# Kernel optimization log

Measured on AMD Instinct MI355X. Metric: run time of the kernel, lower is better.

The kernel has to match this reference:

```python
import jax, jax.numpy as jnp
import numpy as np

PAD = 2  # matches init_kwargs padding

# HEALPix face layout (DLWP-HEALPix / earth2grid convention):
#   faces 0-3 : northern polar cap
#   faces 4-7 : equatorial belt
#   faces 8-11: southern polar cap
# Padding each face gathers edge strips from topological neighbor faces;
# polar-cap neighbors require 90/180-degree rotations, and the two degenerate
# equatorial corners (touching a pole vertex, 3 faces meet) are filled with
# edge continuations + an averaged corner pixel.

def _rot(x, k):
    return jnp.rot90(x, k, axes=(-2, -1))

def _corner_tl(t, l, p):
    # degenerate top-left corner of an equatorial face (pole vertex)
    shp = t.shape[:-2] + (p, p)
    c = jnp.zeros(shp, t.dtype)
    c = c.at[..., :, -1].set(t[..., -p:, 0])          # continue top neighbor's left edge
    c = c.at[..., -1, :].set(l[..., 0, -p:])          # continue left neighbor's top edge
    c = c.at[..., -1, -1].set(0.5 * t[..., -1, 0] + 0.5 * l[..., 0, -1])
    return c

def _corner_br(b, r, p):
    # degenerate bottom-right corner of an equatorial face (pole vertex)
    shp = b.shape[:-2] + (p, p)
    c = jnp.zeros(shp, b.dtype)
    c = c.at[..., :, 0].set(b[..., :p, -1])
    c = c.at[..., 0, :].set(r[..., -1, :p])
    c = c.at[..., 0, 0].set(0.5 * b[..., 0, -1] + 0.5 * r[..., -1, 0])
    return c

def _assemble(tl, t, tr, l, c, r, bl, b, br):
    top = jnp.concatenate([tl, t, tr], axis=-1)
    mid = jnp.concatenate([l, c, r], axis=-1)
    bot = jnp.concatenate([bl, b, br], axis=-1)
    return jnp.concatenate([top, mid, bot], axis=-2)

def _pn(c, t, tl, l, bl, b, br, r, tr, p):
    # northern polar face: top/left neighbors are rotated polar faces
    return _assemble(
        _rot(tl, 2)[..., -p:, -p:], _rot(t, 1)[..., -p:, :], _rot(tr, 1)[..., -p:, :p],
        _rot(l, -1)[..., :, -p:],   c,                       r[..., :, :p],
        bl[..., :p, -p:],           b[..., :p, :],           br[..., :p, :p])

def _pe(c, t, tl, l, bl, b, br, r, tr, p):
    # equatorial face: no rotations; tl/br are precomputed degenerate corners
    return _assemble(
        tl,               t[..., -p:, :], tr[..., -p:, :p],
        l[..., :, -p:],   c,              r[..., :, :p],
        bl[..., :p, -p:], b[..., :p, :],  br)

def _ps(c, t, tl, l, bl, b, br, r, tr, p):
    # southern polar face: mirror image of the northern case
    return _assemble(
        tl[..., -p:, :p], t[..., -p:, :],        tr[..., -p:, -p:],
        l[..., :, -p:],   c,                     _rot(r, -1)[..., :, :p],
        _rot(bl, 1)[..., :p, -p:], _rot(b, 1)[..., :p, :], _rot(br, 2)[..., :p, :p])

def healpix_pad(x, p):
    # x: (B, 12, C, H, W) -> (B, 12, C, H+2p, W+2p)
    f = [x[:, i] for i in range(12)]
    out = []
    for i in range(4):  # northern cap faces 0..3
        out.append(_pn(f[i], t=f[(i + 1) % 4], tl=f[(i + 2) % 4], l=f[(i - 1) % 4],
                       bl=f[(i - 1) % 4], b=f[4 + i], br=f[8 + i],
                       r=f[4 + (i + 1) % 4], tr=f[(i + 1) % 4], p=p))
    for i in range(4):  # equatorial faces 4..7
        out.append(_pe(f[4 + i], t=f[i], tl=_corner_tl(f[i], f[(i - 1) % 4], p),
                       l=f[(i - 1) % 4], bl=f[4 + (i - 1) % 4], b=f[8 + i],
                       br=_corner_br(f[8 + i], f[8 + (i - 1) % 4], p),
                       r=f[4 + (i + 1) % 4], tr=f[i], p=p))
    for i in range(4):  # southern cap faces 8..11
        out.append(_ps(f[8 + i], t=f[4 + i], tl=f[4 + i], l=f[4 + (i + 1) % 4],
                       bl=f[8 + (i + 1) % 4], b=f[8 + (i - 1) % 4], br=f[8 + (i - 1) % 4],
                       r=f[8 + (i + 1) % 4], tr=f[i], p=p))
    return jnp.stack(out, axis=1)


def setup_inputs() -> dict:
    key = jax.random.key(0)
    x = jax.random.normal(key, (2, 12, 32, 256, 256), dtype=jnp.float32)
    return {"x": x}


def reference(x) -> jnp.ndarray:
    return healpix_pad(x, PAD)
```

## Files before the change

### kernel.cpp

```cpp
#include <hip/hip_runtime.h>


constexpr int N  = 256;
constexpr int P  = 2;
constexpr int NP = N + 2 * P;
constexpr int C  = 32;
constexpr int PLANE_OUT = NP * NP;
constexpr int PLANE_IN  = N * N;
constexpr int BULK_X    = 32;

typedef float f32x4 __attribute__((ext_vector_type(4)));

__device__ __forceinline__ float gather(const float* __restrict__ in,
                                        int basePlane, int face, int i,
                                        int oh, int ow) {
    auto L = [&](int f, int sh, int sw) -> float {
        return in[(size_t)(basePlane + f * C) * PLANE_IN + sh * N + sw];
    };

    float v;
    if (face < 4) {
        if (oh < P) {
            if (ow < P)              v = L((i + 2) & 3, P - 1 - oh, P - 1 - ow);
            else if (ow < P + N)     v = L((i + 1) & 3, ow - P, P - 1 - oh);
            else                     v = L((i + 1) & 3, ow - P - N, P - 1 - oh);
        } else if (oh < P + N) {
            int ch = oh - P;
            if (ow < P)              v = L((i + 3) & 3, P - 1 - ow, ch);
            else if (ow < P + N)     v = L(face, ch, ow - P);
            else                     v = L(4 + ((i + 1) & 3), ch, ow - P - N);
        } else {
            int bh = oh - P - N;
            if (ow < P)              v = L((i + 3) & 3, bh, N - P + ow);
            else if (ow < P + N)     v = L(4 + i, bh, ow - P);
            else                     v = L(8 + i, bh, ow - P - N);
        }
    } else if (face < 8) {
        if (oh < P) {
            if (ow < P) {
                if (oh == P - 1 && ow == P - 1)
                    v = 0.5f * L(i, N - 1, 0) + 0.5f * L((i + 3) & 3, 0, N - 1);
                else if (oh == P - 1) v = L((i + 3) & 3, 0, N - P + ow);
                else if (ow == P - 1) v = L(i, N - P + oh, 0);
                else                  v = 0.0f;
            }
            else if (ow < P + N)     v = L(i, N - P + oh, ow - P);
            else                     v = L(i, N - P + oh, ow - P - N);
        } else if (oh < P + N) {
            int ch = oh - P;
            if (ow < P)              v = L((i + 3) & 3, ch, N - P + ow);
            else if (ow < P + N)     v = L(face, ch, ow - P);
            else                     v = L(4 + ((i + 1) & 3), ch, ow - P - N);
        } else {
            int bh = oh - P - N;
            if (ow < P)              v = L(4 + ((i + 3) & 3), bh, N - P + ow);
            else if (ow < P + N)     v = L(8 + i, bh, ow - P);
            else {
                int bw = ow - P - N;
                if (bh == 0 && bw == 0)
                    v = 0.5f * L(8 + i, 0, N - 1) + 0.5f * L(8 + ((i + 3) & 3), N - 1, 0);
                else if (bh == 0)     v = L(8 + ((i + 3) & 3), N - 1, bw);
                else if (bw == 0)     v = L(8 + i, bh, N - 1);
                else                  v = 0.0f;
            }
        }
    } else {
        if (oh < P) {
            if (ow < P)              v = L(4 + i, N - P + oh, ow);
            else if (ow < P + N)     v = L(4 + i, N - P + oh, ow - P);
            else                     v = L(i, N - P + oh, N - P + (ow - P - N));
        } else if (oh < P + N) {
            int ch = oh - P;
            if (ow < P)              v = L(4 + ((i + 1) & 3), ch, N - P + ow);
            else if (ow < P + N)     v = L(face, ch, ow - P);
            else {
                int bw = ow - P - N;
                v = L(8 + ((i + 1) & 3), N - 1 - bw, ch);
            }
        } else {
            int bh = oh - P - N;
            if (ow < P)              v = L(8 + ((i + 1) & 3), N - P + ow, N - 1 - bh);
            else if (ow < P + N)     v = L(8 + ((i + 3) & 3), ow - P, N - 1 - bh);
            else {
                int bw = ow - P - N;
                v = L(8 + ((i + 3) & 3), N - 1 - bh, N - 1 - bw);
            }
        }
    }
    return v;
}

__global__ __launch_bounds__(256)
void healpix_pad_kernel(const float* __restrict__ in, float* __restrict__ out) {
    const int plane = blockIdx.y;
    const int x     = blockIdx.x;

    float* __restrict__ oplane = out + (size_t)plane * PLANE_OUT;
    const float* __restrict__ iplane = in + (size_t)plane * PLANE_IN;

    const int bc   = plane >> 5;
    const int face = bc >= 12 ? bc - 12 : bc;
    const int i    = face & 3;
    const int basePlane = plane - face * C;

    if (x < BULK_X) {
        const int w = threadIdx.x >> 6;
        const int l = threadIdx.x & 63;
        const int r0 = x * 8 + w;

        #pragma unroll
        for (int k = 0; k < 2; ++k) {
            const int r  = r0 + 4 * k;
            const int oh = r + P;
            const float* __restrict__ src = iplane + r * N;
            float* __restrict__ dst = oplane + oh * NP;

            if (l != 0) {
                float2 a = *reinterpret_cast<const float2*>(src + 4 * l - 2);
                float2 b = *reinterpret_cast<const float2*>(src + 4 * l);
                f32x4 v = {a.x, a.y, b.x, b.y};
                __builtin_nontemporal_store(v, reinterpret_cast<f32x4*>(dst + 4 * l));
            } else {
                f32x4 v0;
                v0.x = gather(in, basePlane, face, i, oh, 0);
                v0.y = gather(in, basePlane, face, i, oh, 1);
                float2 a = *reinterpret_cast<const float2*>(src);
                v0.z = a.x; v0.w = a.y;
                __builtin_nontemporal_store(v0, reinterpret_cast<f32x4*>(dst));
                f32x4 v1;
                float2 b = *reinterpret_cast<const float2*>(src + N - 2);
                v1.x = b.x; v1.y = b.y;
                v1.z = gather(in, basePlane, face, i, oh, NP - 2);
                v1.w = gather(in, basePlane, face, i, oh, NP - 1);
                __builtin_nontemporal_store(v1, reinterpret_cast<f32x4*>(dst + N));
            }
        }
        return;
    }

    for (int t = threadIdx.x; t < 4 * 65; t += 256) {
        int q   = t / 65;
        int row = (q < 2) ? q : 256 + q;
        int j   = t - q * 65;
        int ow  = 4 * j;
        f32x4 v;
        v.x = gather(in, basePlane, face, i, row, ow);
        v.y = gather(in, basePlane, face, i, row, ow + 1);
        v.z = gather(in, basePlane, face, i, row, ow + 2);
        v.w = gather(in, basePlane, face, i, row, ow + 3);
        __builtin_nontemporal_store(v, reinterpret_cast<f32x4*>(oplane + row * NP + ow));
    }
}

extern "C" void kernel_launch(void* const* d_in, const int* in_sizes, int n_in,
                              void* d_out, int out_size, void* d_ws, size_t ws_size,
                              hipStream_t stream) {
    const float* in = (const float*)d_in[0];
    float* out = (float*)d_out;
    int planes = out_size / PLANE_OUT;
    dim3 block(256);
    dim3 grid(BULK_X + 1, planes);
    healpix_pad_kernel<<<grid, block, 0, stream>>>(in, out);
}
```

Measured before the change: 76.56 us.

## Assign contiguous 4-row output chunks per wavefront, flattening bulk and halo paths

Work is repartitioned so that each wavefront owns 4 consecutive output rows (260 float4 stores) and walks them with a flattened index. This replaces the old split between 32 bulk blocks of interior rows and one extra block per plane for the halo rows. The aim is contiguous store streams per wave and removal of the serialized edge-row block that handled gather-heavy rows alone. In exchange it adds per-element divisions and branches, and the last block of each plane has 3 idle wavefronts.

New measurement: 72.15 us. 5.8% less time.

```diff
diff --git a/kernel.cpp b/kernel.cpp
--- a/kernel.cpp
+++ b/kernel.cpp
@@ -7,7 +7,6 @@
 constexpr int C  = 32;
 constexpr int PLANE_OUT = NP * NP;
 constexpr int PLANE_IN  = N * N;
-constexpr int BULK_X    = 32;
 
 typedef float f32x4 __attribute__((ext_vector_type(4)));
 
@@ -93,7 +92,9 @@
 __global__ __launch_bounds__(256)
 void healpix_pad_kernel(const float* __restrict__ in, float* __restrict__ out) {
     const int plane = blockIdx.y;
-    const int x     = blockIdx.x;
+    const int g     = blockIdx.x * 4 + (threadIdx.x >> 6);
+    if (g > 64) return;
+    const int l     = threadIdx.x & 63;
 
     float* __restrict__ oplane = out + (size_t)plane * PLANE_OUT;
     const float* __restrict__ iplane = in + (size_t)plane * PLANE_IN;
@@ -102,52 +103,41 @@
     const int face = bc >= 12 ? bc - 12 : bc;
     const int i    = face & 3;
     const int basePlane = plane - face * C;
+    const int r0   = g * 4;
 
-    if (x < BULK_X) {
-        const int w = threadIdx.x >> 6;
-        const int l = threadIdx.x & 63;
-        const int r0 = x * 8 + w;
+    #pragma unroll
+    for (int it = 0; it < 5; ++it) {
+        const int c = it * 64 + l;
+        if (c >= 260) break;
+        const int q   = c / 65;
+        const int j   = c - q * 65;
+        const int row = r0 + q;
+        const int ow  = 4 * j;
 
-        #pragma unroll
-        for (int k = 0; k < 2; ++k) {
-            const int r  = r0 + 4 * k;
-            const int oh = r + P;
-            const float* __restrict__ src = iplane + r * N;
-            float* __restrict__ dst = oplane + oh * NP;
-
-            if (l != 0) {
-                float2 a = *reinterpret_cast<const float2*>(src + 4 * l - 2);
-                float2 b = *reinterpret_cast<const float2*>(src + 4 * l);
-                f32x4 v = {a.x, a.y, b.x, b.y};
-                __builtin_nontemporal_store(v, reinterpret_cast<f32x4*>(dst + 4 * l));
+        f32x4 v;
+        if (row >= P && row < P + N) {
+            const float* __restrict__ src = iplane + (row - P) * N;
+            if (j == 0) {
+                v.x = gather(in, basePlane, face, i, row, 0);
+                v.y = gather(in, basePlane, face, i, row, 1);
+                float2 a = *reinterpret_cast<const float2*>(src);
+                v.z = a.x; v.w = a.y;
+            } else if (j == 64) {
+                float2 b = *reinterpret_cast<const float2*>(src + N - 2);
+                v.x = b.x; v.y = b.y;
+                v.z = gather(in, basePlane, face, i, row, NP - 2);
+                v.w = gather(in, basePlane, face, i, row, NP - 1);
             } else {
-                f32x4 v0;
-                v0.x = gather(in, basePlane, face, i, oh, 0);
-                v0.y = gather(in, basePlane, face, i, oh, 1);
-                float2 a = *reinterpret_cast<const float2*>(src);
-                v0.z = a.x; v0.w = a.y;
-                __builtin_nontemporal_store(v0, reinterpret_cast<f32x4*>(dst));
-                f32x4 v1;
-                float2 b = *reinterpret_cast<const float2*>(src + N - 2);
-                v1.x = b.x; v1.y = b.y;
-                v1.z = gather(in, basePlane, face, i, oh, NP - 2);
-                v1.w = gather(in, basePlane, face, i, oh, NP - 1);
-                __builtin_nontemporal_store(v1, reinterpret_cast<f32x4*>(dst + N));
+                float2 a = *reinterpret_cast<const float2*>(src + ow - 2);
+                float2 b = *reinterpret_cast<const float2*>(src + ow);
+                v = f32x4{a.x, a.y, b.x, b.y};
             }
+        } else {
+            v.x = gather(in, basePlane, face, i, row, ow);
+            v.y = gather(in, basePlane, face, i, row, ow + 1);
+            v.z = gather(in, basePlane, face, i, row, ow + 2);
+            v.w = gather(in, basePlane, face, i, row, ow + 3);
         }
-        return;
-    }
-
-    for (int t = threadIdx.x; t < 4 * 65; t += 256) {
-        int q   = t / 65;
-        int row = (q < 2) ? q : 256 + q;
-        int j   = t - q * 65;
-        int ow  = 4 * j;
-        f32x4 v;
-        v.x = gather(in, basePlane, face, i, row, ow);
-        v.y = gather(in, basePlane, face, i, row, ow + 1);
-        v.z = gather(in, basePlane, face, i, row, ow + 2);
-        v.w = gather(in, basePlane, face, i, row, ow + 3);
         __builtin_nontemporal_store(v, reinterpret_cast<f32x4*>(oplane + row * NP + ow));
     }
 }
@@ -159,6 +149,6 @@
     float* out = (float*)d_out;
     int planes = out_size / PLANE_OUT;
     dim3 block(256);
-    dim3 grid(BULK_X + 1, planes);
+    dim3 grid(17, planes);
     healpix_pad_kernel<<<grid, block, 0, stream>>>(in, out);
 }
```
